# Performance work log

Measured on AMD Instinct MI355X. Metric: run time of the kernel, lower is better.

The kernel has to match this reference:

```python
import math
import jax, jax.numpy as jnp
import numpy as np

NUM_BUCKETS = 32
MAX_DISTANCE = 128
N_HEADS = 16
D_KV = 64


def relative_position_bucket(rel_pos, num_buckets=NUM_BUCKETS, max_distance=MAX_DISTANCE):
    # bidirectional=True path of the original
    n = -rel_pos
    nb = num_buckets // 2
    ret = (n < 0).astype(jnp.int32) * nb
    n = jnp.abs(n)
    max_exact = nb // 2
    is_small = n < max_exact
    val_large = max_exact + (
        jnp.log(n.astype(jnp.float32) / max_exact)
        / math.log(max_distance / max_exact)
        * (nb - max_exact)
    ).astype(jnp.int32)
    val_large = jnp.minimum(val_large, nb - 1)
    return jnp.where(is_small, n, val_large) + ret


def setup_inputs() -> dict:
    key = jax.random.key(0)
    ks = jax.random.split(key, 6)
    B, S, D = 2, 2048, 1024
    inner = N_HEADS * D_KV  # 1024
    sc = 1.0 / math.sqrt(D)
    return {
        "x": jax.random.normal(ks[0], (B, S, D), dtype=jnp.float32),
        "Wq": jax.random.normal(ks[1], (D, inner), dtype=jnp.float32) * sc,
        "Wk": jax.random.normal(ks[2], (D, inner), dtype=jnp.float32) * sc,
        "Wv": jax.random.normal(ks[3], (D, inner), dtype=jnp.float32) * sc,
        "Wo": jax.random.normal(ks[4], (inner, D), dtype=jnp.float32) * sc,
        "rel_table": jax.random.normal(ks[5], (NUM_BUCKETS, N_HEADS), dtype=jnp.float32),
        "attention_mask": jnp.zeros((B, 1, 1, S), dtype=jnp.float32),
    }


def reference(x, Wq, Wk, Wv, Wo, rel_table, attention_mask):
    B, S, D = x.shape
    H, Dk = N_HEADS, D_KV

    q = (x @ Wq).reshape(B, S, H, Dk).transpose(0, 2, 1, 3)  # bhqd
    k = (x @ Wk).reshape(B, S, H, Dk).transpose(0, 2, 1, 3)
    v = (x @ Wv).reshape(B, S, H, Dk).transpose(0, 2, 1, 3)

    # NOTE: T5 attention has no 1/sqrt(d) scaling
    scores = jnp.einsum('bhqd,bhkd->bhqk', q.astype(jnp.float32), k.astype(jnp.float32))

    pos = jnp.arange(S)
    rel_pos = pos[None, :] - pos[:, None]  # [S,S] = k_pos - q_pos
    buckets = relative_position_bucket(rel_pos)
    position_bias = jnp.transpose(rel_table[buckets], (2, 0, 1))  # [H,S,S]

    scores = scores + position_bias[None, ...] + attention_mask
    weights = jax.nn.softmax(scores, axis=-1)
    out = jnp.einsum('bhqk,bhkd->bhqd', weights, v.astype(jnp.float32))
    out = out.transpose(0, 2, 1, 3).reshape(B, S, H * Dk).astype(x.dtype)
    out = out @ Wo
    return (out, position_bias)
```

## Files before the change

kernel.cpp:

```cpp
#include <hip/hip_runtime.h>
#include <hip/hip_bf16.h>
#include <math.h>
#include <stdint.h>

typedef __bf16 bf16_t;
typedef __attribute__((ext_vector_type(8))) __bf16 bf16x8;
typedef __attribute__((ext_vector_type(4))) float f32x4;
typedef float f32x4a __attribute__((ext_vector_type(4), aligned(4)));
typedef unsigned short u16;
typedef unsigned int u32;

#define DEV static __device__ __forceinline__
#define LOG2E 1.4426950408889634f

DEV u16 f2b(float f){ bf16_t h = (bf16_t)f; return __builtin_bit_cast(u16, h); }
DEV float b2f(u16 u){ bf16_t h = __builtin_bit_cast(bf16_t, u); return (float)h; }
DEV f32x4 mfma16(bf16x8 a, bf16x8 b, f32x4 c){
  return __builtin_amdgcn_mfma_f32_16x16x32_bf16(a, b, c, 0, 0, 0);
}

#if __has_builtin(__builtin_amdgcn_exp2f)
DEV float fexp2(float x){ return __builtin_amdgcn_exp2f(x); }
#else
DEV float fexp2(float x){ return exp2f(x); }
#endif

DEV void gld16(const void* g, void* l){
  __builtin_amdgcn_global_load_lds((const __attribute__((address_space(1))) u32*)g,
                                   (__attribute__((address_space(3))) u32*)l, 16, 0, 0);
}

DEV bf16x8 ldsA64(const u16* arr, int row, int ch){
  return *(const bf16x8*)&arr[row*64 + ((ch ^ (row&7))*8)];
}
DEV bf16x8 ldsA32(const u16* arr, int row, int ch){
  return *(const bf16x8*)&arr[row*32 + ((ch ^ ((row>>1)&3))*8)];
}

__global__ __launch_bounds__(256) void k_prep(const float* __restrict__ x,
                                              const float* __restrict__ Wq, const float* __restrict__ Wk,
                                              const float* __restrict__ Wv, const float* __restrict__ Wo,
                                              const float* __restrict__ rel_table, const float* __restrict__ mask,
                                              u16* __restrict__ xh, u16* __restrict__ xl,
                                              u16* __restrict__ wth, u16* __restrict__ wot,
                                              float* __restrict__ bt, float* __restrict__ bt2,
                                              float* __restrict__ msk2){
  __shared__ float tile[64][65];
  int bid = blockIdx.x;
  int t = threadIdx.x;
  if(bid < 4096){
    size_t i = ((size_t)bid*256 + t)*4;
    float4 v = *(const float4*)(x + i);
    ushort4 hv, lv; float f, hf;
    f=v.x; hv.x=f2b(f); hf=b2f(hv.x); lv.x=f2b(f-hf);
    f=v.y; hv.y=f2b(f); hf=b2f(hv.y); lv.y=f2b(f-hf);
    f=v.z; hv.z=f2b(f); hf=b2f(hv.z); lv.z=f2b(f-hf);
    f=v.w; hv.w=f2b(f); hf=b2f(hv.w); lv.w=f2b(f-hf);
    *(ushort4*)(xh+i) = hv;
    *(ushort4*)(xl+i) = lv;
  } else if(bid < 5120){
    int rr = bid - 4096;
    int z = rr >> 8, ky = (rr >> 4) & 15, nx = rr & 15;
    const float* W = (z==0)?Wq:((z==1)?Wk:((z==2)?Wv:Wo));
    int n0 = nx*64, k0 = ky*64;
    int r = t>>6, c = t&63;
    #pragma unroll
    for(int i=0;i<16;i++){
      int row = i*4 + r;
      tile[row][c] = W[(size_t)(k0+row)*1024 + n0 + c];
    }
    __syncthreads();
    #pragma unroll
    for(int i=0;i<16;i++){
      int nrow = i*4 + r;
      float v = tile[c][nrow];
      size_t o = (size_t)(n0+nrow)*1024 + k0 + c;
      if(z<3) wth[(size_t)z*1048576 + o] = f2b(v);
      else    wot[o] = f2b(v);
    }
  } else {
    int gid = (bid-5120)*256 + t;
    if(gid < 4096) msk2[gid] = mask[gid]*LOG2E;
    int h = gid >> 12, idx = gid & 4095;
    float v = 0.f;
    if(idx < 4095){
      int delta = idx - 2047;
      int n = -delta;
      int ret = 0;
      if(n < 0){ ret = 16; n = -n; }
      int bucket;
      if(n < 8) bucket = n + ret;
      else {
        float a = (float)log((double)n * 0.125);
        float rr2 = (float)((double)a / (double)2.7725887298583984f);
        int vl = 8 + (int)(rr2 * 8.0f);
        vl = vl > 15 ? 15 : vl;
        bucket = vl + ret;
      }
      v = rel_table[bucket*16 + h];
    }
    bt[gid] = v;
    bt2[gid] = v*LOG2E - 32.0f;
  }
}

__global__ __launch_bounds__(256) void k_gemm_qkv(const u16* __restrict__ xh, const u16* __restrict__ xl,
                                                  const u16* __restrict__ wth,
                                                  u16* __restrict__ qh, u16* __restrict__ ql,
                                                  u16* __restrict__ kh, u16* __restrict__ vt){
  __shared__ __align__(16) u16 SM[24576];
  int z = blockIdx.z;
  const u16* WH = wth + (size_t)z*1048576;
  int lin2 = blockIdx.x + 8*blockIdx.y;
  int nl2 = (lin2 & 7)*32 + (lin2 >> 3);
  int n0 = (nl2 & 7)*128, m0 = (nl2 >> 3)*128;
  int t = threadIdx.x, w = t>>6, lane = t&63, l16 = lane&15, g = lane>>4;
  f32x4 acc[4][4];
  #pragma unroll
  for(int i=0;i<4;i++)
    #pragma unroll
    for(int j=0;j<4;j++) acc[i][j] = {0.f,0.f,0.f,0.f};
  int rbase = (w>>1)*64, cbase = (w&1)*64;

  #pragma unroll
  for(int jj=0;jj<6;jj++){
    int q = w + 4*jj;
    int arr = q>>3, sub = q&7;
    if(z!=0 && arr==1) continue;
    int row = sub*16 + (lane>>2);
    int lch = (lane&3) ^ ((row>>1)&3);
    const u16* src;
    if(arr==0)      src = xh + (size_t)(m0+row)*1024 + lch*8;
    else if(arr==1) src = xl + (size_t)(m0+row)*1024 + lch*8;
    else            src = WH + (size_t)(n0+row)*1024 + lch*8;
    gld16(src, &SM[q*512]);
  }
  __syncthreads();

  for(int it=0; it<32; ++it){
    const u16* Ah = SM + (it&1)*12288;
    const u16* Al = Ah + 4096;
    const u16* Bh = Ah + 8192;
    if(it < 31){
      u16* dstb = SM + ((it+1)&1)*12288;
      int kn = (it+1)*32;
      #pragma unroll
      for(int jj=0;jj<6;jj++){
        int q = w + 4*jj;
        int arr = q>>3, sub = q&7;
        if(z!=0 && arr==1) continue;
        int row = sub*16 + (lane>>2);
        int lch = (lane&3) ^ ((row>>1)&3);
        const u16* src;
        if(arr==0)      src = xh + (size_t)(m0+row)*1024 + kn + lch*8;
        else if(arr==1) src = xl + (size_t)(m0+row)*1024 + kn + lch*8;
        else            src = WH + (size_t)(n0+row)*1024 + kn + lch*8;
        gld16(src, dstb + q*512);
      }
      __builtin_amdgcn_sched_barrier(0);
    }
    if(z!=0){
      bf16x8 ah[4];
      #pragma unroll
      for(int i=0;i<4;i++) ah[i] = ldsA32(Ah, rbase + i*16 + l16, g);
      #pragma unroll
      for(int j=0;j<4;j++){
        bf16x8 bh = ldsA32(Bh, cbase + j*16 + l16, g);
        #pragma unroll
        for(int i=0;i<4;i++)
          acc[i][j] = mfma16(ah[i], bh, acc[i][j]);
      }
    } else {
      bf16x8 ah[4], am[4];
      #pragma unroll
      for(int i=0;i<4;i++){
        int row = rbase + i*16 + l16;
        ah[i] = ldsA32(Ah, row, g);
        am[i] = ldsA32(Al, row, g);
      }
      #pragma unroll
      for(int j=0;j<4;j++){
        bf16x8 bh = ldsA32(Bh, cbase + j*16 + l16, g);
        #pragma unroll
        for(int i=0;i<4;i++){
          acc[i][j] = mfma16(ah[i], bh, acc[i][j]);
          acc[i][j] = mfma16(am[i], bh, acc[i][j]);
        }
      }
    }
    __syncthreads();
  }
  if(z==2){
    #pragma unroll
    for(int i=0;i<4;i++)
      #pragma unroll
      for(int j=0;j<4;j++)
        #pragma unroll
        for(int r=0;r<4;r++){
          int ml = rbase + i*16 + g*4 + r;
          int nl = cbase + j*16 + l16;
          SM[nl*136 + ml] = f2b(acc[i][j][r]);
        }
    __syncthreads();
    int bb = m0 >> 11;
    #pragma unroll
    for(int kk=0;kk<8;kk++){
      int id = t + 256*kk;
      int row = id>>4, ch = id&15;
      uint4 v = *(const uint4*)&SM[row*136 + ch*8];
      int n = n0 + row;
      size_t dst = ((size_t)(bb*16 + (n>>6))*64 + (n&63))*2048 + (m0&2047) + ch*8;
      *(uint4*)&vt[dst] = v;
    }
  } else {
    #pragma unroll
    for(int i=0;i<4;i++)
      #pragma unroll
      for(int j=0;j<4;j++)
        #pragma unroll
        for(int r=0;r<4;r++){
          int m = m0 + rbase + i*16 + g*4 + r;
          int n = n0 + cbase + j*16 + l16;
          float v = acc[i][j][r];
          if(z==0) v *= LOG2E;
          int b = m >> 11, s = m & 2047;
          int hh = n >> 6, d = n & 63;
          size_t a = ((size_t)(b*16+hh)*2048 + s)*64 + d;
          u16 hb = f2b(v);
          if(z==0){ qh[a]=hb; ql[a]=f2b(v - b2f(hb)); }
          else    { kh[a]=hb; }
        }
  }
}

__global__ __launch_bounds__(256,4) void k_attn(const u16* __restrict__ qh, const u16* __restrict__ ql,
                                              const u16* __restrict__ kh,
                                              const u16* __restrict__ vt, const float* __restrict__ bt2,
                                              const float* __restrict__ msk2,
                                              const float* __restrict__ bt, float* __restrict__ bias_out,
                                              u16* __restrict__ ao){
  __shared__ __align__(16) u16 SM[20480];
  int lin = blockIdx.x + 32*blockIdx.y;
  int nlw = (lin & 7)*128 + (lin >> 3);
  int qx = nlw & 31, bh = nlw >> 5;
  int b = bh>>4, h = bh&15;
  int q0 = qx*64;
  int t = threadIdx.x, w = t>>6, lane = t&63, l16 = lane&15, g = lane>>4;
  size_t base  = (size_t)bh*2048*64;
  size_t vbase = (size_t)bh*64*2048;
  u16* PSw = SM + 16384 + w*1024;
  const float* bt2h = bt2 + h*4096;
  const float* msk2b = msk2 + b*2048;
  size_t wbase = ((size_t)(bh*32 + qx))*65536 + t*8;

  bf16x8 qfh[2], qfl[2];
  {
    int qr = q0 + w*16 + l16;
    size_t a0 = base + (size_t)qr*64 + g*8;
    qfh[0] = *(const bf16x8*)&qh[a0];
    qfl[0] = *(const bf16x8*)&ql[a0];
    qfh[1] = *(const bf16x8*)&qh[a0+32];
    qfl[1] = *(const bf16x8*)&ql[a0+32];
  }
  f32x4 O[4];
  float rs4[4];
  #pragma unroll
  for(int jd=0;jd<4;jd++) O[jd] = {0.f,0.f,0.f,0.f};
  #pragma unroll
  for(int r=0;r<4;r++) rs4[r] = 0.f;
  int qgbase = q0 + w*16 + g*4;

  f32x4a bv0, bv1;
  {
    size_t f = wbase;
    int hh = (int)(f >> 22);
    int rem = (int)(f & 4194303);
    int qq = rem >> 11;
    int kk = rem & 2047;
    const float* row = bt + hh*4096 + (kk - qq + 2047);
    bv0 = *(const f32x4a*)(row);
    bv1 = *(const f32x4a*)(row + 4);
  }
  #pragma unroll
  for(int jj=0;jj<4;jj++){
    int q = w + 4*jj;
    int arr = q>>3, sub = q&7;
    int row = sub*8 + (lane>>3);
    int lch = (lane&7) ^ (row&7);
    const u16* src = (arr==0) ? kh + base + (size_t)row*64 + lch*8
                              : vt + vbase + (size_t)row*2048 + lch*8;
    gld16(src, &SM[q*512]);
  }
  __syncthreads();

  for(int it=0; it<32; ++it){
    int k0 = it*64;
    const u16* KH = SM + (it&1)*8192;
    const u16* VT = KH + 4096;
    if(it < 31){
      u16* dstb = SM + ((it+1)&1)*8192;
      int kn = k0 + 64;
      #pragma unroll
      for(int jj=0;jj<4;jj++){
        int q = w + 4*jj;
        int arr = q>>3, sub = q&7;
        int row = sub*8 + (lane>>3);
        int lch = (lane&7) ^ (row&7);
        const u16* src = (arr==0) ? kh + base + (size_t)(kn+row)*64 + lch*8
                                  : vt + vbase + (size_t)row*2048 + kn + lch*8;
        gld16(src, dstb + q*512);
      }
      __builtin_amdgcn_sched_barrier(0);
    }
    f32x4 sc[4];
    {
      const float* bb = bt2h + (k0 + g*4 + 2047 - (q0 + w*16 + l16));
      const float* mm = msk2b + k0 + g*4;
      #pragma unroll
      for(int j=0;j<4;j++){
        f32x4a bvv = *(const f32x4a*)(bb + j*16);
        f32x4a mvv = *(const f32x4a*)(mm + j*16);
        sc[j] = (f32x4){bvv[0]+mvv[0], bvv[1]+mvv[1], bvv[2]+mvv[2], bvv[3]+mvv[3]};
      }
    }
    {
      size_t f = wbase + (size_t)it*2048;
      __builtin_nontemporal_store(bv0, (f32x4a*)(bias_out + f));
      __builtin_nontemporal_store(bv1, (f32x4a*)(bias_out + f + 4));
      if(it < 31){
        size_t fn = f + 2048;
        int hh = (int)(fn >> 22);
        int rem = (int)(fn & 4194303);
        int qq = rem >> 11;
        int kk = rem & 2047;
        const float* row = bt + hh*4096 + (kk - qq + 2047);
        bv0 = *(const f32x4a*)(row);
        bv1 = *(const f32x4a*)(row + 4);
      }
    }
    __builtin_amdgcn_s_setprio(1);
    #pragma unroll
    for(int j=0;j<4;j++){
      int krow = j*16 + l16;
      bf16x8 kfh0 = ldsA64(KH, krow, g);
      bf16x8 kfh1 = ldsA64(KH, krow, 4+g);
      f32x4 s = sc[j];
      s = mfma16(kfh0, qfh[0], s);
      s = mfma16(kfh0, qfl[0], s);
      s = mfma16(kfh1, qfh[1], s);
      s = mfma16(kfh1, qfl[1], s);
      sc[j] = s;
    }
    __builtin_amdgcn_s_setprio(0);
    #pragma unroll
    for(int j=0;j<4;j++){
      float p0 = fexp2(sc[j][0]); rs4[0] += p0;
      float p1 = fexp2(sc[j][1]); rs4[1] += p1;
      float p2 = fexp2(sc[j][2]); rs4[2] += p2;
      float p3 = fexp2(sc[j][3]); rs4[3] += p3;
      ushort4 us = { f2b(p0), f2b(p1), f2b(p2), f2b(p3) };
      int ch = (j*2 + (g>>1)) ^ (l16 & 7);
      *(ushort4*)&PSw[l16*64 + ch*8 + (g&1)*4] = us;
    }
    __builtin_amdgcn_s_setprio(1);
    #pragma unroll
    for(int ds=0; ds<2; ds++){
      bf16x8 pa = ldsA64(PSw, l16, ds*4 + g);
      #pragma unroll
      for(int jd=0;jd<4;jd++){
        bf16x8 vb = ldsA64(VT, jd*16 + l16, ds*4 + g);
        O[jd] = mfma16(pa, vb, O[jd]);
      }
    }
    __builtin_amdgcn_s_setprio(0);
    __syncthreads();
  }
  float tot = (rs4[0]+rs4[1]) + (rs4[2]+rs4[3]);
  tot += __shfl_xor(tot, 16, 64);
  tot += __shfl_xor(tot, 32, 64);
  #pragma unroll
  for(int r=0;r<4;r++){
    float inv = 1.f/__shfl(tot, g*4+r, 64);
    int q = qgbase + r;
    size_t a = ((size_t)(b*2048 + q))*1024 + h*64;
    #pragma unroll
    for(int jd=0;jd<4;jd++)
      ao[a + jd*16 + l16] = f2b(O[jd][r]*inv);
  }
}

__global__ __launch_bounds__(256) void k_gemm_out(const u16* __restrict__ ao, const u16* __restrict__ wot,
                                                  float* __restrict__ out){
  __shared__ __align__(16) u16 SM[12288];
  int lin2 = blockIdx.x + 16*blockIdx.y;
  int nl2 = (lin2 & 7)*64 + (lin2 >> 3);
  int n0 = (nl2 & 15)*64, m0 = (nl2 >> 4)*128;
  int t = threadIdx.x, w = t>>6, lane = t&63, l16 = lane&15, g = lane>>4;
  f32x4 acc[4][2];
  #pragma unroll
  for(int i=0;i<4;i++)
    #pragma unroll
    for(int j=0;j<2;j++) acc[i][j] = {0.f,0.f,0.f,0.f};
  int rbase = (w>>1)*64, cbase = (w&1)*32;

  #pragma unroll
  for(int jj=0;jj<3;jj++){
    int q = w + 4*jj;
    int arr = q>>3, sub = q&7;
    int row = sub*16 + (lane>>2);
    int lch = (lane&3) ^ ((row>>1)&3);
    const u16* src = (arr==0) ? ao  + (size_t)(m0+row)*1024 + lch*8
                              : wot + (size_t)(n0+row)*1024 + lch*8;
    gld16(src, &SM[q*512]);
  }
  __syncthreads();

  for(int it=0; it<32; ++it){
    const u16* As = SM + (it&1)*6144;
    const u16* Bs = As + 4096;
    if(it < 31){
      u16* dstb = SM + ((it+1)&1)*6144;
      int kn = (it+1)*32;
      #pragma unroll
      for(int jj=0;jj<3;jj++){
        int q = w + 4*jj;
        int arr = q>>3, sub = q&7;
        int row = sub*16 + (lane>>2);
        int lch = (lane&3) ^ ((row>>1)&3);
        const u16* src = (arr==0) ? ao  + (size_t)(m0+row)*1024 + kn + lch*8
                                  : wot + (size_t)(n0+row)*1024 + kn + lch*8;
        gld16(src, dstb + q*512);
      }
      __builtin_amdgcn_sched_barrier(0);
    }
    bf16x8 af[4];
    #pragma unroll
    for(int i=0;i<4;i++) af[i] = ldsA32(As, rbase + i*16 + l16, g);
    #pragma unroll
    for(int j=0;j<2;j++){
      bf16x8 bfb = ldsA32(Bs, cbase + j*16 + l16, g);
      #pragma unroll
      for(int i=0;i<4;i++)
        acc[i][j] = mfma16(af[i], bfb, acc[i][j]);
    }
    __syncthreads();
  }
  #pragma unroll
  for(int i=0;i<4;i++)
    #pragma unroll
    for(int j=0;j<2;j++)
      #pragma unroll
      for(int r=0;r<4;r++){
        int m = m0 + rbase + i*16 + g*4 + r;
        int n = n0 + cbase + j*16 + l16;
        __builtin_nontemporal_store(acc[i][j][r], &out[(size_t)m*1024 + n]);
      }
}

extern "C" void kernel_launch(void* const* d_in, const int* in_sizes, int n_in,
                              void* d_out, int out_size, void* d_ws, size_t ws_size,
                              hipStream_t stream) {
  const float* x   = (const float*)d_in[0];
  const float* Wq  = (const float*)d_in[1];
  const float* Wk  = (const float*)d_in[2];
  const float* Wv  = (const float*)d_in[3];
  const float* Wo  = (const float*)d_in[4];
  const float* rel = (const float*)d_in[5];
  const float* msk = (const float*)d_in[6];
  float* out = (float*)d_out;
  float* bias_out = out + (size_t)4194304;
  char* ws = (char*)d_ws;
  u16* xh  = (u16*)(ws + 0);
  u16* xl  = (u16*)(ws + 8388608);
  u16* wth = (u16*)(ws + 16777216);
  u16* wot = (u16*)(ws + 23068672);
  u16* qh  = (u16*)(ws + 25165824);
  u16* ql  = (u16*)(ws + 33554432);
  u16* kh  = (u16*)(ws + 41943040);
  u16* vt  = (u16*)(ws + 50331648);
  u16* ao  = (u16*)(ws + 58720256);
  float* bt  = (float*)(ws + 67108864);
  float* bt2 = (float*)(ws + 67371008);
  float* msk2= (float*)(ws + 67633152);

  k_prep      <<<5376, 256, 0, stream>>>(x, Wq, Wk, Wv, Wo, rel, msk,
                                         xh, xl, wth, wot, bt, bt2, msk2);
  k_gemm_qkv  <<<dim3(8,32,3), 256, 0, stream>>>(xh, xl, wth, qh, ql, kh, vt);
  k_attn      <<<dim3(32,32), 256, 0, stream>>>(qh, ql, kh, vt, bt2, msk2, bt, bias_out, ao);
  k_gemm_out  <<<dim3(16,32), 256, 0, stream>>>(ao, wot, out);
}
```

Before: 435.9 us.

## Retile attention waves as a 2x2 grid over query rows and key columns

Each of the four waves in the attention kernel now covers 32 query rows and one 32-key half of each key tile, instead of 16 query rows over all 64 keys. Each K and V fragment read from LDS then feeds two query tiles, cutting LDS read traffic per MFMA. The two key-half partial outputs and row sums are combined through shared memory at the end before normalisation. The position-bias output load is no longer prefetched one iteration ahead. It also doubles the Q fragment registers per wave and adds an extra barrier and reduction step.

Result: slower. 454.3 us (+4.2%).

```diff
diff --git a/kernel.cpp b/kernel.cpp
--- a/kernel.cpp
+++ b/kernel.cpp
@@ -246,41 +246,31 @@
   int b = bh>>4, h = bh&15;
   int q0 = qx*64;
   int t = threadIdx.x, w = t>>6, lane = t&63, l16 = lane&15, g = lane>>4;
+  int wr = w>>1, wc = w&1;
   size_t base  = (size_t)bh*2048*64;
   size_t vbase = (size_t)bh*64*2048;
-  u16* PSw = SM + 16384 + w*1024;
+  u16* PSq = SM + 16384 + w*1024;
   const float* bt2h = bt2 + h*4096;
   const float* msk2b = msk2 + b*2048;
   size_t wbase = ((size_t)(bh*32 + qx))*65536 + t*8;
 
-  bf16x8 qfh[2], qfl[2];
-  {
-    int qr = q0 + w*16 + l16;
+  bf16x8 qfh[2][2], qfl[2][2];
+  #pragma unroll
+  for(int jq=0;jq<2;jq++){
+    int qr = q0 + wr*32 + jq*16 + l16;
     size_t a0 = base + (size_t)qr*64 + g*8;
-    qfh[0] = *(const bf16x8*)&qh[a0];
-    qfl[0] = *(const bf16x8*)&ql[a0];
-    qfh[1] = *(const bf16x8*)&qh[a0+32];
-    qfl[1] = *(const bf16x8*)&ql[a0+32];
-  }
-  f32x4 O[4];
-  float rs4[4];
-  #pragma unroll
-  for(int jd=0;jd<4;jd++) O[jd] = {0.f,0.f,0.f,0.f};
-  #pragma unroll
-  for(int r=0;r<4;r++) rs4[r] = 0.f;
-  int qgbase = q0 + w*16 + g*4;
-
-  f32x4a bv0, bv1;
-  {
-    size_t f = wbase;
-    int hh = (int)(f >> 22);
-    int rem = (int)(f & 4194303);
-    int qq = rem >> 11;
-    int kk = rem & 2047;
-    const float* row = bt + hh*4096 + (kk - qq + 2047);
-    bv0 = *(const f32x4a*)(row);
-    bv1 = *(const f32x4a*)(row + 4);
-  }
+    qfh[jq][0] = *(const bf16x8*)&qh[a0];
+    qfl[jq][0] = *(const bf16x8*)&ql[a0];
+    qfh[jq][1] = *(const bf16x8*)&qh[a0+32];
+    qfl[jq][1] = *(const bf16x8*)&ql[a0+32];
+  }
+  f32x4 O[2][4];
+  float rsw[2] = {0.f, 0.f};
+  #pragma unroll
+  for(int jq=0;jq<2;jq++)
+    #pragma unroll
+    for(int jd=0;jd<4;jd++) O[jq][jd] = {0.f,0.f,0.f,0.f};
+
   #pragma unroll
   for(int jj=0;jj<4;jj++){
     int q = w + 4*jj;
@@ -312,80 +302,123 @@
       }
       __builtin_amdgcn_sched_barrier(0);
     }
-    f32x4 sc[4];
-    {
-      const float* bb = bt2h + (k0 + g*4 + 2047 - (q0 + w*16 + l16));
-      const float* mm = msk2b + k0 + g*4;
-      #pragma unroll
-      for(int j=0;j<4;j++){
-        f32x4a bvv = *(const f32x4a*)(bb + j*16);
-        f32x4a mvv = *(const f32x4a*)(mm + j*16);
-        sc[j] = (f32x4){bvv[0]+mvv[0], bvv[1]+mvv[1], bvv[2]+mvv[2], bvv[3]+mvv[3]};
-      }
-    }
     {
       size_t f = wbase + (size_t)it*2048;
-      __builtin_nontemporal_store(bv0, (f32x4a*)(bias_out + f));
-      __builtin_nontemporal_store(bv1, (f32x4a*)(bias_out + f + 4));
-      if(it < 31){
-        size_t fn = f + 2048;
-        int hh = (int)(fn >> 22);
-        int rem = (int)(fn & 4194303);
-        int qq = rem >> 11;
-        int kk = rem & 2047;
-        const float* row = bt + hh*4096 + (kk - qq + 2047);
-        bv0 = *(const f32x4a*)(row);
-        bv1 = *(const f32x4a*)(row + 4);
-      }
+      int hh = (int)(f >> 22);
+      int rem = (int)(f & 4194303);
+      int qq = rem >> 11;
+      int kk = rem & 2047;
+      const float* row = bt + hh*4096 + (kk - qq + 2047);
+      f32x4a v0 = *(const f32x4a*)(row);
+      f32x4a v1 = *(const f32x4a*)(row + 4);
+      __builtin_nontemporal_store(v0, (f32x4a*)(bias_out + f));
+      __builtin_nontemporal_store(v1, (f32x4a*)(bias_out + f + 4));
+    }
+    f32x4 sc[2][2];
+    {
+      int kb = k0 + wc*32 + g*4;
+      const float* mm = msk2b + kb;
+      const float* bb = bt2h + (kb + 2047 - (q0 + wr*32 + l16));
+      #pragma unroll
+      for(int jq=0;jq<2;jq++)
+        #pragma unroll
+        for(int j=0;j<2;j++){
+          f32x4a bvv = *(const f32x4a*)(bb + j*16 - jq*16);
+          f32x4a mvv = *(const f32x4a*)(mm + j*16);
+          sc[jq][j] = (f32x4){bvv[0]+mvv[0], bvv[1]+mvv[1], bvv[2]+mvv[2], bvv[3]+mvv[3]};
+        }
     }
     __builtin_amdgcn_s_setprio(1);
     #pragma unroll
-    for(int j=0;j<4;j++){
-      int krow = j*16 + l16;
+    for(int j=0;j<2;j++){
+      int krow = wc*32 + j*16 + l16;
       bf16x8 kfh0 = ldsA64(KH, krow, g);
       bf16x8 kfh1 = ldsA64(KH, krow, 4+g);
-      f32x4 s = sc[j];
-      s = mfma16(kfh0, qfh[0], s);
-      s = mfma16(kfh0, qfl[0], s);
-      s = mfma16(kfh1, qfh[1], s);
-      s = mfma16(kfh1, qfl[1], s);
-      sc[j] = s;
+      #pragma unroll
+      for(int jq=0;jq<2;jq++){
+        f32x4 s = sc[jq][j];
+        s = mfma16(kfh0, qfh[jq][0], s);
+        s = mfma16(kfh0, qfl[jq][0], s);
+        s = mfma16(kfh1, qfh[jq][1], s);
+        s = mfma16(kfh1, qfl[jq][1], s);
+        sc[jq][j] = s;
+      }
     }
     __builtin_amdgcn_s_setprio(0);
     #pragma unroll
-    for(int j=0;j<4;j++){
-      float p0 = fexp2(sc[j][0]); rs4[0] += p0;
-      float p1 = fexp2(sc[j][1]); rs4[1] += p1;
-      float p2 = fexp2(sc[j][2]); rs4[2] += p2;
-      float p3 = fexp2(sc[j][3]); rs4[3] += p3;
-      ushort4 us = { f2b(p0), f2b(p1), f2b(p2), f2b(p3) };
-      int ch = (j*2 + (g>>1)) ^ (l16 & 7);
-      *(ushort4*)&PSw[l16*64 + ch*8 + (g&1)*4] = us;
-    }
+    for(int jq=0;jq<2;jq++)
+      #pragma unroll
+      for(int j=0;j<2;j++){
+        float p0 = fexp2(sc[jq][j][0]);
+        float p1 = fexp2(sc[jq][j][1]);
+        float p2 = fexp2(sc[jq][j][2]);
+        float p3 = fexp2(sc[jq][j][3]);
+        rsw[jq] += (p0+p1) + (p2+p3);
+        ushort4 us = { f2b(p0), f2b(p1), f2b(p2), f2b(p3) };
+        int rowp = jq*16 + l16;
+        int c8 = j*2 + (g>>1);
+        *(ushort4*)&PSq[rowp*32 + ((c8 ^ ((rowp>>1)&3))*8) + (g&1)*4] = us;
+      }
     __builtin_amdgcn_s_setprio(1);
-    #pragma unroll
-    for(int ds=0; ds<2; ds++){
-      bf16x8 pa = ldsA64(PSw, l16, ds*4 + g);
-      #pragma unroll
-      for(int jd=0;jd<4;jd++){
-        bf16x8 vb = ldsA64(VT, jd*16 + l16, ds*4 + g);
-        O[jd] = mfma16(pa, vb, O[jd]);
+    {
+      bf16x8 vbh[4];
+      #pragma unroll
+      for(int jd=0;jd<4;jd++) vbh[jd] = ldsA64(VT, jd*16 + l16, wc*4 + g);
+      #pragma unroll
+      for(int jq=0;jq<2;jq++){
+        bf16x8 pa = ldsA32(PSq, jq*16 + l16, g);
+        #pragma unroll
+        for(int jd=0;jd<4;jd++)
+          O[jq][jd] = mfma16(pa, vbh[jd], O[jq][jd]);
       }
     }
     __builtin_amdgcn_s_setprio(0);
     __syncthreads();
   }
-  float tot = (rs4[0]+rs4[1]) + (rs4[2]+rs4[3]);
-  tot += __shfl_xor(tot, 16, 64);
-  tot += __shfl_xor(tot, 32, 64);
-  #pragma unroll
-  for(int r=0;r<4;r++){
-    float inv = 1.f/__shfl(tot, g*4+r, 64);
-    int q = qgbase + r;
-    size_t a = ((size_t)(b*2048 + q))*1024 + h*64;
-    #pragma unroll
-    for(int jd=0;jd<4;jd++)
-      ao[a + jd*16 + l16] = f2b(O[jd][r]*inv);
+
+  float* Of = (float*)SM;
+  if(wc == 1){
+    #pragma unroll
+    for(int jq=0;jq<2;jq++)
+      #pragma unroll
+      for(int jd=0;jd<4;jd++){
+        int c = jq*4 + jd;
+        *(f32x4*)&Of[wr*2048 + lane*32 + ((c ^ (lane&7))*4)] = O[jq][jd];
+      }
+    float* rsf = (float*)&SM[16384 + w*1024];
+    rsf[lane] = rsw[0];
+    rsf[64+lane] = rsw[1];
+  }
+  __syncthreads();
+  if(wc == 0){
+    float* rsf = (float*)&SM[16384 + (w+1)*1024];
+    float tot0 = rsw[0] + rsf[lane];
+    float tot1 = rsw[1] + rsf[64+lane];
+    tot0 += __shfl_xor(tot0, 16, 64);
+    tot0 += __shfl_xor(tot0, 32, 64);
+    tot1 += __shfl_xor(tot1, 16, 64);
+    tot1 += __shfl_xor(tot1, 32, 64);
+    #pragma unroll
+    for(int jq=0;jq<2;jq++)
+      #pragma unroll
+      for(int jd=0;jd<4;jd++){
+        int c = jq*4 + jd;
+        f32x4 part = *(const f32x4*)&Of[wr*2048 + lane*32 + ((c ^ (lane&7))*4)];
+        O[jq][jd] += part;
+      }
+    #pragma unroll
+    for(int jq=0;jq<2;jq++){
+      float tj = (jq==0) ? tot0 : tot1;
+      #pragma unroll
+      for(int r=0;r<4;r++){
+        float inv = 1.f/__shfl(tj, g*4+r, 64);
+        int q = q0 + wr*32 + jq*16 + g*4 + r;
+        size_t a = ((size_t)(b*2048 + q))*1024 + h*64;
+        #pragma unroll
+        for(int jd=0;jd<4;jd++)
+          ao[a + jd*16 + l16] = f2b(O[jq][jd][r]*inv);
+      }
+    }
   }
 }
 
```
